# Kernel optimization log

Hardware: AMD Instinct MI355X
Metric: run time of the kernel (lower is better)

Reference implementation:

```python
import jax, jax.numpy as jnp
import numpy as np

QMAX = 127.0


def setup_inputs() -> dict:
    key = jax.random.key(0)
    k1, k2, k3, k4, k5, k6 = jax.random.split(key, 6)
    B, IN, OUT = 8192, 4096, 4096
    # Quantized activation (uint8-range values stored as float, per-sample asymmetric quant)
    x_q = jax.random.randint(k1, (B, IN), 0, 256).astype(jnp.float32)
    x_scale = jax.random.uniform(k2, (B,), dtype=jnp.float32, minval=0.001, maxval=0.02)
    x_zp = jax.random.randint(k3, (B,), 0, 256).astype(jnp.float32)
    # Symmetric per-tensor int8 weight (values in [-127, 127]) + scalar scale
    w_q = jax.random.randint(k4, (OUT, IN), -127, 128).astype(jnp.float32)
    w_scale = jax.random.uniform(k5, (1,), dtype=jnp.float32, minval=0.001, maxval=0.02)
    fp_bias = jax.random.normal(k6, (OUT,), dtype=jnp.float32)
    return {"x_q": x_q, "x_scale": x_scale, "x_zp": x_zp, "w_q": w_q,
            "w_scale": w_scale, "fp_bias": fp_bias}


def reference(x_q, x_scale, x_zp, w_q, w_scale, fp_bias):
    # zero-point subtraction (per-sample)
    xt = x_q - x_zp[:, None]                      # [B, IN]
    # integer GEMM (values are integers held in float32)
    lin = xt @ w_q.T                              # [B, OUT]
    # integer bias: round(fp_bias / (w_scale * x_scale))
    qbias = jnp.round(fp_bias[None, :] / (w_scale[0] * x_scale[:, None]))  # [B, OUT]
    lin = lin + qbias
    # requantize: symmetric per-tensor int8
    s = jnp.max(jnp.abs(lin)) / QMAX
    q = jnp.clip(jnp.round(lin / s), -QMAX, QMAX)  # [B, OUT]
    out_scale = s * x_scale * w_scale[0]           # [B]
    zero_point = jnp.zeros_like(out_scale)
    return q, out_scale, zero_point
```

## Files before the change

### kernel.cpp

```cpp
#include <hip/hip_runtime.h>
#include <hip/hip_bf16.h>


typedef int i32x4 __attribute__((ext_vector_type(4)));

#define AS1 __attribute__((address_space(1)))
#define AS3 __attribute__((address_space(3)))

__device__ __forceinline__ void async16(const void* g, void* lds) {
    __builtin_amdgcn_global_load_lds((const AS1 void*)g, (AS3 void*)lds, 16, 0, 0);
}

__global__ void conv_x_kernel(const float4* __restrict__ xq, int* __restrict__ x8,
                              int* gmax, int n4) {
    int i = blockIdx.x * 256 + threadIdx.x;
    if (i == 0) *gmax = 0;
    if (i >= n4) return;
    float4 v = xq[i];
    int b0 = ((int)v.x - 128) & 255;
    int b1 = ((int)v.y - 128) & 255;
    int b2 = ((int)v.z - 128) & 255;
    int b3 = ((int)v.w - 128) & 255;
    x8[i] = b0 | (b1 << 8) | (b2 << 16) | (b3 << 24);
}

__global__ void conv_w_kernel(const float* __restrict__ wq, int* __restrict__ w8,
                              int* __restrict__ rowsum, int K) {
    int row = blockIdx.x;
    int t = threadIdx.x;
    const float4* src = (const float4*)(wq + (size_t)row * K);
    int* dst = w8 + (size_t)row * (K >> 2);
    int sum = 0;
    int passes = K >> 10;
    for (int p = 0; p < passes; ++p) {
        float4 v = src[p * 256 + t];
        int b0 = (int)v.x, b1 = (int)v.y, b2 = (int)v.z, b3 = (int)v.w;
        sum += b0 + b1 + b2 + b3;
        dst[p * 256 + t] = (b0 & 255) | ((b1 & 255) << 8) | ((b2 & 255) << 16) | ((b3 & 255) << 24);
    }
    #pragma unroll
    for (int m = 32; m; m >>= 1) sum += __shfl_xor(sum, m, 64);
    __shared__ int wsum[4];
    if ((t & 63) == 0) wsum[t >> 6] = sum;
    __syncthreads();
    if (t == 0) rowsum[row] = wsum[0] + wsum[1] + wsum[2] + wsum[3];
}

__global__ __launch_bounds__(256, 3) void gemm_i8_kernel(
    const char* __restrict__ x8, const char* __restrict__ w8,
    const int* __restrict__ w_rowsum,
    const float* __restrict__ x_scale, const float* __restrict__ x_zp,
    const float* __restrict__ fp_bias, const float* __restrict__ w_scale_p,
    int* __restrict__ lin_out, int* gmax, int N, int K) {
    __shared__ __align__(16) char lds[3][16384];
    __shared__ int s_bmax;

    const int t = threadIdx.x;
    const int w = t >> 6, l = t & 63;
    if (t == 0) s_bmax = 0;

    const int nwg = gridDim.x;
    int swz = blockIdx.x;
    if ((nwg & 7) == 0) { const int cpx = nwg >> 3; swz = (swz & 7) * cpx + (swz >> 3); }
    const int ntn = N >> 7;
    const int tm = swz / ntn, tn = swz % ntn;

    const int nt = K >> 6;

    const int srow = t >> 2;
    const int phys = (t & 3) ^ ((srow >> 1) & 3);
    const char* pA0 = x8 + (size_t)(tm * 128 + srow) * K + phys * 16;
    const char* pA1 = pA0 + (size_t)64 * K;
    const char* pB0 = w8 + (size_t)(tn * 128 + srow) * K + phys * 16;
    const char* pB1 = pB0 + (size_t)64 * K;
    const int dst_t = t * 16;

    const int lane_lo = l & 15, lane_hi = l >> 4;
    const int wm = w >> 1, wn = w & 1;
    const int ar = wm * 64 + lane_lo;
    const int aoff = ar * 64 + ((lane_hi ^ ((ar >> 1) & 3)) << 4);
    const int br = wn * 64 + lane_lo;
    const int boff = 8192 + br * 64 + ((lane_hi ^ ((br >> 1) & 3)) << 4);

    i32x4 acc[4][4] = {};

    #pragma unroll
    for (int g = 0; g < 2; ++g) {
        char* buf = lds[g];
        const size_t koff = (size_t)g * 64;
        async16(pA0 + koff, buf + dst_t);
        async16(pA1 + koff, buf + 4096 + dst_t);
        async16(pB0 + koff, buf + 8192 + dst_t);
        async16(pB1 + koff, buf + 12288 + dst_t);
    }

    int cur = 0, stg = 2;
    for (int j = 0; j < nt; ++j) {
        if (j + 1 < nt) asm volatile("s_waitcnt vmcnt(4)" ::: "memory");
        else            asm volatile("s_waitcnt vmcnt(0)" ::: "memory");
        __builtin_amdgcn_s_barrier();
        if (j + 2 < nt) {
            char* sb = lds[stg];
            const size_t koff = (size_t)(j + 2) << 6;
            async16(pA0 + koff, sb + dst_t);
            async16(pA1 + koff, sb + 4096 + dst_t);
            async16(pB0 + koff, sb + 8192 + dst_t);
            async16(pB1 + koff, sb + 12288 + dst_t);
        }
        const char* buf = lds[cur];
        i32x4 af[4], bf[4];
        #pragma unroll
        for (int n = 0; n < 4; ++n) bf[n] = *(const i32x4*)(buf + boff + n * 1024);
        #pragma unroll
        for (int m = 0; m < 4; ++m) af[m] = *(const i32x4*)(buf + aoff + m * 1024);
        __builtin_amdgcn_s_setprio(1);
        #pragma unroll
        for (int m = 0; m < 4; ++m)
            #pragma unroll
            for (int n = 0; n < 4; ++n)
                acc[m][n] = __builtin_amdgcn_mfma_i32_16x16x64_i8(af[m], bf[n], acc[m][n], 0, 0, 0);
        __builtin_amdgcn_s_setprio(0);
        cur = (cur == 2) ? 0 : cur + 1;
        stg = (stg == 2) ? 0 : stg + 1;
    }

    const float ws = *w_scale_p;
    const int rowg0 = tm * 128 + wm * 64 + lane_hi * 4;
    const int colg0 = tn * 128 + wn * 64 + lane_lo;
    float fbws[4]; int wrs[4];
    #pragma unroll
    for (int n = 0; n < 4; ++n) {
        fbws[n] = fp_bias[colg0 + n * 16] / ws;
        wrs[n] = w_rowsum[colg0 + n * 16];
    }
    int lmax = 0;
    #pragma unroll
    for (int m = 0; m < 4; ++m) {
        #pragma unroll
        for (int r = 0; r < 4; ++r) {
            const int row = rowg0 + m * 16 + r;
            const float rxs = 1.0f / x_scale[row];
            const int zz = 128 - (int)x_zp[row];
            int* orow = lin_out + (size_t)row * N + colg0;
            #pragma unroll
            for (int n = 0; n < 4; ++n) {
                const int qb = (int)rintf(fbws[n] * rxs);
                const int lin = acc[m][n][r] + zz * wrs[n] + qb;
                const int a = lin < 0 ? -lin : lin;
                lmax = a > lmax ? a : lmax;
                orow[n * 16] = lin;
            }
        }
    }
    atomicMax(&s_bmax, lmax);
    __syncthreads();
    if (t == 0) atomicMax(gmax, s_bmax);
}

__global__ void requant_kernel(float4* qout, const int4* lin, const int* gmax, int n4) {
    int i = blockIdx.x * 256 + threadIdx.x;
    if (i >= n4) return;
    float s = (float)(*gmax) / 127.0f;
    int4 v = lin[i];
    float4 o;
    o.x = fminf(127.0f, fmaxf(-127.0f, rintf((float)v.x / s)));
    o.y = fminf(127.0f, fmaxf(-127.0f, rintf((float)v.y / s)));
    o.z = fminf(127.0f, fmaxf(-127.0f, rintf((float)v.z / s)));
    o.w = fminf(127.0f, fmaxf(-127.0f, rintf((float)v.w / s)));
    qout[i] = o;
}

__global__ void scale_kernel(float* __restrict__ out_scale, float* __restrict__ out_zp,
                             const float* __restrict__ x_scale,
                             const float* __restrict__ w_scale_p,
                             const int* gmax, int B) {
    int i = blockIdx.x * 256 + threadIdx.x;
    if (i >= B) return;
    float s = (float)(*gmax) / 127.0f;
    out_scale[i] = s * x_scale[i] * w_scale_p[0];
    out_zp[i] = 0.0f;
}

extern "C" void kernel_launch(void* const* d_in, const int* in_sizes, int n_in,
                              void* d_out, int out_size, void* d_ws, size_t ws_size,
                              hipStream_t stream) {
    const float* x_q     = (const float*)d_in[0];
    const float* x_scale = (const float*)d_in[1];
    const float* x_zp    = (const float*)d_in[2];
    const float* w_q     = (const float*)d_in[3];
    const float* w_scale = (const float*)d_in[4];
    const float* fp_bias = (const float*)d_in[5];

    const int B   = in_sizes[1];
    const int IN  = in_sizes[0] / B;
    const int OUT = in_sizes[5];

    float* q         = (float*)d_out;
    float* out_scale = q + (size_t)B * OUT;
    float* out_zp    = out_scale + B;

    char* ws    = (char*)d_ws;
    int* gmax   = (int*)ws;
    char* x8    = ws + 64;
    char* w8    = x8 + (size_t)B * IN;
    int* rowsum = (int*)(w8 + (size_t)OUT * IN);
    size_t needed = 64 + (size_t)B * IN + (size_t)OUT * IN + (size_t)OUT * 4;
    if (ws_size < needed) return;

    int n4x = (B * IN) >> 2;
    conv_x_kernel<<<(n4x + 255) / 256, 256, 0, stream>>>((const float4*)x_q, (int*)x8, gmax, n4x);
    conv_w_kernel<<<OUT, 256, 0, stream>>>(w_q, (int*)w8, rowsum, IN);

    int nblocks = (B / 128) * (OUT / 128);
    gemm_i8_kernel<<<nblocks, 256, 0, stream>>>(x8, w8, rowsum, x_scale, x_zp, fp_bias,
                                                w_scale, (int*)q, gmax, OUT, IN);

    int n4q = (B * OUT) >> 2;
    requant_kernel<<<(n4q + 255) / 256, 256, 0, stream>>>((float4*)q, (const int4*)q, gmax, n4q);
    scale_kernel<<<(B + 255) / 256, 256, 0, stream>>>(out_scale, out_zp, x_scale, w_scale, gmax, B);
}
```

Baseline: 277.6 us.

## Load B operand directly from global into registers, bypassing LDS staging

The weight (B) tiles are no longer staged through shared memory. Each lane now loads its MFMA B fragments straight from global memory into registers, prefetched one K-step ahead. LDS use drops to half and B-side LDS reads are gone, but B data is no longer shared: both waves with the same wn fetch identical fragments, so global/L2 traffic for B doubles. The vmcnt wait counts are retuned to cover the extra in-flight register loads, and the change adds register pressure.

```diff
diff --git a/kernel.cpp b/kernel.cpp
--- a/kernel.cpp
+++ b/kernel.cpp
@@ -52,7 +52,7 @@
     const float* __restrict__ x_scale, const float* __restrict__ x_zp,
     const float* __restrict__ fp_bias, const float* __restrict__ w_scale_p,
     int* __restrict__ lin_out, int* gmax, int N, int K) {
-    __shared__ __align__(16) char lds[3][16384];
+    __shared__ __align__(16) char lds[3][8192];
     __shared__ int s_bmax;
 
     const int t = threadIdx.x;
@@ -71,46 +71,46 @@
     const int phys = (t & 3) ^ ((srow >> 1) & 3);
     const char* pA0 = x8 + (size_t)(tm * 128 + srow) * K + phys * 16;
     const char* pA1 = pA0 + (size_t)64 * K;
-    const char* pB0 = w8 + (size_t)(tn * 128 + srow) * K + phys * 16;
-    const char* pB1 = pB0 + (size_t)64 * K;
     const int dst_t = t * 16;
 
     const int lane_lo = l & 15, lane_hi = l >> 4;
     const int wm = w >> 1, wn = w & 1;
     const int ar = wm * 64 + lane_lo;
     const int aoff = ar * 64 + ((lane_hi ^ ((ar >> 1) & 3)) << 4);
-    const int br = wn * 64 + lane_lo;
-    const int boff = 8192 + br * 64 + ((lane_hi ^ ((br >> 1) & 3)) << 4);
+
+    const char* pB = w8 + (size_t)(tn * 128 + wn * 64 + lane_lo) * K + lane_hi * 16;
+    const size_t bstep = (size_t)16 * K;
 
     i32x4 acc[4][4] = {};
+    i32x4 bf[4], bfn[4];
 
     #pragma unroll
     for (int g = 0; g < 2; ++g) {
-        char* buf = lds[g];
         const size_t koff = (size_t)g * 64;
-        async16(pA0 + koff, buf + dst_t);
-        async16(pA1 + koff, buf + 4096 + dst_t);
-        async16(pB0 + koff, buf + 8192 + dst_t);
-        async16(pB1 + koff, buf + 12288 + dst_t);
-    }
+        async16(pA0 + koff, lds[g] + dst_t);
+        async16(pA1 + koff, lds[g] + 4096 + dst_t);
+    }
+    #pragma unroll
+    for (int n = 0; n < 4; ++n) bf[n] = *(const i32x4*)(pB + n * bstep);
 
     int cur = 0, stg = 2;
     for (int j = 0; j < nt; ++j) {
-        if (j + 1 < nt) asm volatile("s_waitcnt vmcnt(4)" ::: "memory");
-        else            asm volatile("s_waitcnt vmcnt(0)" ::: "memory");
+        if (j + 1 < nt) asm volatile("s_waitcnt vmcnt(6)" ::: "memory");
+        else            asm volatile("s_waitcnt vmcnt(4)" ::: "memory");
         __builtin_amdgcn_s_barrier();
         if (j + 2 < nt) {
-            char* sb = lds[stg];
             const size_t koff = (size_t)(j + 2) << 6;
-            async16(pA0 + koff, sb + dst_t);
-            async16(pA1 + koff, sb + 4096 + dst_t);
-            async16(pB0 + koff, sb + 8192 + dst_t);
-            async16(pB1 + koff, sb + 12288 + dst_t);
+            async16(pA0 + koff, lds[stg] + dst_t);
+            async16(pA1 + koff, lds[stg] + 4096 + dst_t);
+        }
+        if (j + 1 < nt) {
+            const size_t koff = (size_t)(j + 1) << 6;
+            #pragma unroll
+            for (int n = 0; n < 4; ++n)
+                bfn[n] = *(const i32x4*)(pB + n * bstep + koff);
         }
         const char* buf = lds[cur];
-        i32x4 af[4], bf[4];
-        #pragma unroll
-        for (int n = 0; n < 4; ++n) bf[n] = *(const i32x4*)(buf + boff + n * 1024);
+        i32x4 af[4];
         #pragma unroll
         for (int m = 0; m < 4; ++m) af[m] = *(const i32x4*)(buf + aoff + m * 1024);
         __builtin_amdgcn_s_setprio(1);
@@ -120,6 +120,10 @@
             for (int n = 0; n < 4; ++n)
                 acc[m][n] = __builtin_amdgcn_mfma_i32_16x16x64_i8(af[m], bf[n], acc[m][n], 0, 0, 0);
         __builtin_amdgcn_s_setprio(0);
+        if (j + 1 < nt) {
+            #pragma unroll
+            for (int n = 0; n < 4; ++n) bf[n] = bfn[n];
+        }
         cur = (cur == 2) ? 0 : cur + 1;
         stg = (stg == 2) ? 0 : stg + 1;
     }
```

Result: slower. 379.5 us (+36.7%).

## Pre-tile int8 operands in MFMA fragment layout and load directly to registers

Applied to the files above, without the earlier changes.

The conversion kernels now emit x and w in a tiled layout where each lane's 16-byte MFMA fragment is contiguous per 64-wide k tile. The GEMM drops the LDS triple-buffered async copy pipeline and barriers, and instead loads fragments from global memory into registers with a two-stage software double buffer. A separate rowsum kernel recomputes weight row sums from the tiled int8 data. This removes LDS traffic and block-level syncs, but each wave now fetches its operands independently from cache rather than sharing them through LDS, which raises global and L2 load pressure.

```diff
diff --git a/kernel.cpp b/kernel.cpp
--- a/kernel.cpp
+++ b/kernel.cpp
@@ -4,57 +4,80 @@
 
 typedef int i32x4 __attribute__((ext_vector_type(4)));
 
-#define AS1 __attribute__((address_space(1)))
-#define AS3 __attribute__((address_space(3)))
-
-__device__ __forceinline__ void async16(const void* g, void* lds) {
-    __builtin_amdgcn_global_load_lds((const AS1 void*)g, (AS3 void*)lds, 16, 0, 0);
-}
-
-__global__ void conv_x_kernel(const float4* __restrict__ xq, int* __restrict__ x8,
-                              int* gmax, int n4) {
-    int i = blockIdx.x * 256 + threadIdx.x;
-    if (i == 0) *gmax = 0;
-    if (i >= n4) return;
-    float4 v = xq[i];
-    int b0 = ((int)v.x - 128) & 255;
-    int b1 = ((int)v.y - 128) & 255;
-    int b2 = ((int)v.z - 128) & 255;
-    int b3 = ((int)v.w - 128) & 255;
-    x8[i] = b0 | (b1 << 8) | (b2 << 16) | (b3 << 24);
-}
-
-__global__ void conv_w_kernel(const float* __restrict__ wq, int* __restrict__ w8,
-                              int* __restrict__ rowsum, int K) {
-    int row = blockIdx.x;
-    int t = threadIdx.x;
-    const float4* src = (const float4*)(wq + (size_t)row * K);
-    int* dst = w8 + (size_t)row * (K >> 2);
+__global__ void conv_x_kernel(const float* __restrict__ xq, char* __restrict__ x8t,
+                              int* gmax, int IN) {
+    const int nkt = IN >> 6;
+    const int bm = blockIdx.x / nkt, kt = blockIdx.x % nkt;
+    const int t = threadIdx.x;
+    const int m = t >> 6, l = t & 63;
+    if (blockIdx.x == 0 && t == 0) *gmax = 0;
+    const int row = bm * 128 + m * 16 + (l & 15);
+    const int col = kt * 64 + (l >> 4) * 16;
+    const float4* src = (const float4*)(xq + (size_t)row * IN + col);
+    uint out[4];
+    #pragma unroll
+    for (int c = 0; c < 4; ++c) {
+        float4 v = src[c];
+        out[c] = (((int)v.x - 128) & 255) | ((((int)v.y - 128) & 255) << 8) |
+                 ((((int)v.z - 128) & 255) << 16) | ((((int)v.w - 128) & 255) << 24);
+    }
+    *(uint4*)(x8t + ((size_t)blockIdx.x * 8 + m) * 1024 + l * 16) =
+        make_uint4(out[0], out[1], out[2], out[3]);
+}
+
+__global__ void conv_w_kernel(const float* __restrict__ wq, char* __restrict__ w8t,
+                              int IN) {
+    const int nkt = IN >> 6;
+    const int bn = blockIdx.x / nkt, kt = blockIdx.x % nkt;
+    const int t = threadIdx.x;
+    const int m = t >> 6, l = t & 63;
+    const int row = bn * 128 + m * 16 + (l & 15);
+    const int col = kt * 64 + (l >> 4) * 16;
+    const float4* src = (const float4*)(wq + (size_t)row * IN + col);
+    uint out[4];
+    #pragma unroll
+    for (int c = 0; c < 4; ++c) {
+        float4 v = src[c];
+        out[c] = (((int)v.x) & 255) | ((((int)v.y) & 255) << 8) |
+                 ((((int)v.z) & 255) << 16) | ((((int)v.w) & 255) << 24);
+    }
+    *(uint4*)(w8t + ((size_t)blockIdx.x * 8 + m) * 1024 + l * 16) =
+        make_uint4(out[0], out[1], out[2], out[3]);
+}
+
+__global__ void rowsum_kernel(const char* __restrict__ w8t, int* __restrict__ rowsum,
+                              int IN) {
+    const int r = blockIdx.x;
+    const int bn = r >> 7, n = (r >> 4) & 7, rl = r & 15;
+    const int t = threadIdx.x;
+    const int nkt = IN >> 6;
     int sum = 0;
-    int passes = K >> 10;
-    for (int p = 0; p < passes; ++p) {
-        float4 v = src[p * 256 + t];
-        int b0 = (int)v.x, b1 = (int)v.y, b2 = (int)v.z, b3 = (int)v.w;
-        sum += b0 + b1 + b2 + b3;
-        dst[p * 256 + t] = (b0 & 255) | ((b1 & 255) << 8) | ((b2 & 255) << 16) | ((b3 & 255) << 24);
-    }
-    #pragma unroll
-    for (int m = 32; m; m >>= 1) sum += __shfl_xor(sum, m, 64);
+    for (int idx = t; idx < nkt * 4; idx += 256) {
+        const int kt = idx >> 2, cs = idx & 3;
+        const int* p = (const int*)(w8t + (((size_t)bn * nkt + kt) * 8 + n) * 1024
+                                    + (size_t)((cs << 4) | rl) * 16);
+        #pragma unroll
+        for (int k = 0; k < 4; ++k) {
+            const int u = p[k];
+            sum += ((int)(u << 24) >> 24) + ((int)(u << 16) >> 24) +
+                   ((int)(u << 8) >> 24) + (u >> 24);
+        }
+    }
+    #pragma unroll
+    for (int msk = 32; msk; msk >>= 1) sum += __shfl_xor(sum, msk, 64);
     __shared__ int wsum[4];
     if ((t & 63) == 0) wsum[t >> 6] = sum;
     __syncthreads();
-    if (t == 0) rowsum[row] = wsum[0] + wsum[1] + wsum[2] + wsum[3];
+    if (t == 0) rowsum[r] = wsum[0] + wsum[1] + wsum[2] + wsum[3];
 }
 
 __global__ __launch_bounds__(256, 3) void gemm_i8_kernel(
-    const char* __restrict__ x8, const char* __restrict__ w8,
+    const char* __restrict__ x8t, const char* __restrict__ w8t,
     const int* __restrict__ w_rowsum,
     const float* __restrict__ x_scale, const float* __restrict__ x_zp,
     const float* __restrict__ fp_bias, const float* __restrict__ w_scale_p,
     int* __restrict__ lin_out, int* gmax, int N, int K) {
-    __shared__ __align__(16) char lds[3][16384];
     __shared__ int s_bmax;
-
     const int t = threadIdx.x;
     const int w = t >> 6, l = t & 63;
     if (t == 0) s_bmax = 0;
@@ -66,63 +89,41 @@
     const int tm = swz / ntn, tn = swz % ntn;
 
     const int nt = K >> 6;
-
-    const int srow = t >> 2;
-    const int phys = (t & 3) ^ ((srow >> 1) & 3);
-    const char* pA0 = x8 + (size_t)(tm * 128 + srow) * K + phys * 16;
-    const char* pA1 = pA0 + (size_t)64 * K;
-    const char* pB0 = w8 + (size_t)(tn * 128 + srow) * K + phys * 16;
-    const char* pB1 = pB0 + (size_t)64 * K;
-    const int dst_t = t * 16;
-
     const int lane_lo = l & 15, lane_hi = l >> 4;
     const int wm = w >> 1, wn = w & 1;
-    const int ar = wm * 64 + lane_lo;
-    const int aoff = ar * 64 + ((lane_hi ^ ((ar >> 1) & 3)) << 4);
-    const int br = wn * 64 + lane_lo;
-    const int boff = 8192 + br * 64 + ((lane_hi ^ ((br >> 1) & 3)) << 4);
+
+    const char* pa = x8t + ((size_t)tm * nt * 8 + (size_t)wm * 4) * 1024 + l * 16;
+    const char* pb = w8t + ((size_t)tn * nt * 8 + (size_t)wn * 4) * 1024 + l * 16;
 
     i32x4 acc[4][4] = {};
-
-    #pragma unroll
-    for (int g = 0; g < 2; ++g) {
-        char* buf = lds[g];
-        const size_t koff = (size_t)g * 64;
-        async16(pA0 + koff, buf + dst_t);
-        async16(pA1 + koff, buf + 4096 + dst_t);
-        async16(pB0 + koff, buf + 8192 + dst_t);
-        async16(pB1 + koff, buf + 12288 + dst_t);
-    }
-
-    int cur = 0, stg = 2;
-    for (int j = 0; j < nt; ++j) {
-        if (j + 1 < nt) asm volatile("s_waitcnt vmcnt(4)" ::: "memory");
-        else            asm volatile("s_waitcnt vmcnt(0)" ::: "memory");
-        __builtin_amdgcn_s_barrier();
-        if (j + 2 < nt) {
-            char* sb = lds[stg];
-            const size_t koff = (size_t)(j + 2) << 6;
-            async16(pA0 + koff, sb + dst_t);
-            async16(pA1 + koff, sb + 4096 + dst_t);
-            async16(pB0 + koff, sb + 8192 + dst_t);
-            async16(pB1 + koff, sb + 12288 + dst_t);
-        }
-        const char* buf = lds[cur];
-        i32x4 af[4], bf[4];
-        #pragma unroll
-        for (int n = 0; n < 4; ++n) bf[n] = *(const i32x4*)(buf + boff + n * 1024);
-        #pragma unroll
-        for (int m = 0; m < 4; ++m) af[m] = *(const i32x4*)(buf + aoff + m * 1024);
-        __builtin_amdgcn_s_setprio(1);
-        #pragma unroll
-        for (int m = 0; m < 4; ++m)
-            #pragma unroll
-            for (int n = 0; n < 4; ++n)
-                acc[m][n] = __builtin_amdgcn_mfma_i32_16x16x64_i8(af[m], bf[n], acc[m][n], 0, 0, 0);
-        __builtin_amdgcn_s_setprio(0);
-        cur = (cur == 2) ? 0 : cur + 1;
-        stg = (stg == 2) ? 0 : stg + 1;
-    }
+    i32x4 aA[4], bA[4], aB[4], bB[4];
+
+    #define LDA(dst, j) { const char* p_ = pa + (size_t)(j) * 8192;                 \
+        dst[0] = *(const i32x4*)(p_);        dst[1] = *(const i32x4*)(p_ + 1024);   \
+        dst[2] = *(const i32x4*)(p_ + 2048); dst[3] = *(const i32x4*)(p_ + 3072); }
+    #define LDB(dst, j) { const char* p_ = pb + (size_t)(j) * 8192;                 \
+        dst[0] = *(const i32x4*)(p_);        dst[1] = *(const i32x4*)(p_ + 1024);   \
+        dst[2] = *(const i32x4*)(p_ + 2048); dst[3] = *(const i32x4*)(p_ + 3072); }
+    #define MFMA16(a_, b_) {                                                        \
+        __builtin_amdgcn_s_setprio(1);                                              \
+        _Pragma("unroll")                                                           \
+        for (int m = 0; m < 4; ++m)                                                 \
+            _Pragma("unroll")                                                       \
+            for (int n = 0; n < 4; ++n)                                             \
+                acc[m][n] = __builtin_amdgcn_mfma_i32_16x16x64_i8(a_[m], b_[n],     \
+                                                                  acc[m][n], 0,0,0);\
+        __builtin_amdgcn_s_setprio(0); }
+
+    LDA(aA, 0); LDB(bA, 0);
+    for (int j = 0; j < nt; j += 2) {
+        LDA(aB, j + 1); LDB(bB, j + 1);
+        MFMA16(aA, bA);
+        if (j + 2 < nt) { LDA(aA, j + 2); LDB(bA, j + 2); }
+        MFMA16(aB, bB);
+    }
+    #undef LDA
+    #undef LDB
+    #undef MFMA16
 
     const float ws = *w_scale_p;
     const int rowg0 = tm * 128 + wm * 64 + lane_hi * 4;
@@ -152,6 +153,7 @@
             }
         }
     }
+    __syncthreads();
     atomicMax(&s_bmax, lmax);
     __syncthreads();
     if (t == 0) atomicMax(gmax, s_bmax);
@@ -201,18 +203,18 @@
 
     char* ws    = (char*)d_ws;
     int* gmax   = (int*)ws;
-    char* x8    = ws + 64;
-    char* w8    = x8 + (size_t)B * IN;
-    int* rowsum = (int*)(w8 + (size_t)OUT * IN);
+    char* x8t   = ws + 64;
+    char* w8t   = x8t + (size_t)B * IN;
+    int* rowsum = (int*)(w8t + (size_t)OUT * IN);
     size_t needed = 64 + (size_t)B * IN + (size_t)OUT * IN + (size_t)OUT * 4;
     if (ws_size < needed) return;
 
-    int n4x = (B * IN) >> 2;
-    conv_x_kernel<<<(n4x + 255) / 256, 256, 0, stream>>>((const float4*)x_q, (int*)x8, gmax, n4x);
-    conv_w_kernel<<<OUT, 256, 0, stream>>>(w_q, (int*)w8, rowsum, IN);
+    conv_x_kernel<<<(B / 128) * (IN / 64), 512, 0, stream>>>(x_q, x8t, gmax, IN);
+    conv_w_kernel<<<(OUT / 128) * (IN / 64), 512, 0, stream>>>(w_q, w8t, IN);
+    rowsum_kernel<<<OUT, 256, 0, stream>>>(w8t, rowsum, IN);
 
     int nblocks = (B / 128) * (OUT / 128);
-    gemm_i8_kernel<<<nblocks, 256, 0, stream>>>(x8, w8, rowsum, x_scale, x_zp, fp_bias,
+    gemm_i8_kernel<<<nblocks, 256, 0, stream>>>(x8t, w8t, rowsum, x_scale, x_zp, fp_bias,
                                                 w_scale, (int*)q, gmax, OUT, IN);
 
     int n4q = (B * OUT) >> 2;
```

Result: slower. 307.3 us (+10.7%).
